# Kernel tuning notes

Measured on AMD Instinct MI355X. Metric: run time of the kernel, lower is better.

## Reference

```python
import jax, jax.numpy as jnp
import numpy as np

TOP_K = 2
LORA_SCALE = 32.0 / 16.0  # alpha / rank


def setup_inputs() -> dict:
    key = jax.random.key(0)
    ks = jax.random.split(key, 11)
    N, D, F, E, R = 1024, 2048, 5632, 8, 16
    s = lambda k, shape, fan: jax.random.normal(k, shape, jnp.float32) / np.sqrt(fan)
    return {
        "x": jax.random.normal(ks[0], (N, D), jnp.float32),
        "gate_w": s(ks[1], (E, D), D),
        "W1": s(ks[2], (F, D), D),
        "W3": s(ks[3], (F, D), D),
        "W2": s(ks[4], (D, F), F),
        "A1": s(ks[5], (E, R, D), D),
        "B1": s(ks[6], (F, R), R)[None].repeat(E, 0) * 0.0 + s(ks[6], (E, F, R), R),
        "A3": s(ks[7], (E, R, D), D),
        "B3": s(ks[8], (E, F, R), R),
        "A2": s(ks[9], (E, R, F), F),
        "B2": s(ks[10], (E, D, R), R),
    }


def reference(x, gate_w, W1, W3, W2, A1, B1, A3, B3, A2, B2):
    # --- router: softmax over experts, top-k, renormalized combine weights ---
    logits = x @ gate_w.T                                   # [N, E]
    probs = jax.nn.softmax(logits, axis=-1)
    topw, topi = jax.lax.top_k(probs, TOP_K)                # [N, K]
    topw = topw / jnp.sum(topw, axis=-1, keepdims=True)
    E = gate_w.shape[0]
    w = jnp.sum(jax.nn.one_hot(topi, E, dtype=x.dtype) * topw[..., None], axis=1)  # [N, E]

    # --- experts: shared base weights + per-expert LoRA (fused SwiGLU) ---
    base1 = x @ W1.T                                        # [N, F]
    base3 = x @ W3.T                                        # [N, F]
    l1 = jnp.einsum("nd,erd->ner", x, A1)                   # rank-R bottleneck
    l3 = jnp.einsum("nd,erd->ner", x, A3)
    h1 = base1[:, None, :] + LORA_SCALE * jnp.einsum("ner,efr->nef", l1, B1)  # [N, E, F]
    h3 = base3[:, None, :] + LORA_SCALE * jnp.einsum("ner,efr->nef", l3, B3)
    s = jax.nn.silu(h1) * h3                                # [N, E, F]

    # down-projection: shared W2 applied to the routed mixture, plus per-expert LoRA
    s_mix = jnp.einsum("ne,nef->nf", w, s)                  # [N, F]
    out = s_mix @ W2.T                                      # [N, D]
    l2 = jnp.einsum("nef,erf->ner", s, A2) * (w[:, :, None] * LORA_SCALE)
    out = out + jnp.einsum("ner,edr->nd", l2, B2)           # [N, D]
    return out, logits
```

## Files before the change

### kernel.cpp

```cpp
#include <hip/hip_runtime.h>

typedef unsigned int u32;
typedef unsigned short u16;

#define N_TOK 1024
#define D_DIM 2048
#define F_DIM 5632
#define E_NUM 8
#define R_DIM 16
#define LSCALE 2.0f
#define FT 256
#define NT (F_DIM / FT)
#define TC 8
#define BN13 11520
#define ZSPLIT 8

typedef __bf16 bf16x8 __attribute__((ext_vector_type(8)));
typedef float f32x4 __attribute__((ext_vector_type(4)));
typedef u16 u16x8 __attribute__((ext_vector_type(8)));

__device__ inline u16 f2bf(float f) {
    u32 u = __builtin_bit_cast(u32, f);
    u32 r = (u + 0x7fffu + ((u >> 16) & 1u)) >> 16;
    return (u16)r;
}
__device__ inline float bf2f(u16 h) {
    u32 u = ((u32)h) << 16;
    return __builtin_bit_cast(float, u);
}

#define LGKM0() do { asm volatile("s_waitcnt lgkmcnt(0)" ::: "memory"); \
                     __builtin_amdgcn_sched_barrier(0); } while (0)
#define VMC(n)  do { asm volatile("s_waitcnt vmcnt(" #n ")" ::: "memory"); \
                     __builtin_amdgcn_sched_barrier(0); } while (0)

__global__ __launch_bounds__(256) void cvt_all(const float* __restrict__ x,
                                               const float* __restrict__ W1,
                                               const float* __restrict__ W3,
                                               const float* __restrict__ A1,
                                               const float* __restrict__ A3,
                                               const float* __restrict__ W2,
                                               const float* __restrict__ B1,
                                               const float* __restrict__ B3,
                                               u16* __restrict__ xb,
                                               u16* __restrict__ w13,
                                               u16* __restrict__ w2b,
                                               u16* __restrict__ b1b,
                                               u16* __restrict__ b3b) {
    int i = blockIdx.x * 256 + threadIdx.x;
    const float* src;
    u16* dst;
    int off;
    if (i < 524288)       { src = x;  dst = xb;             off = i; }
    else if (i < 3407872) { src = W1; dst = w13;            off = i - 524288; }
    else if (i < 6291456) { src = W3; dst = w13 + 11534336; off = i - 3407872; }
    else if (i < 6356992) { src = A1; dst = w13 + 23068672; off = i - 6291456; }
    else if (i < 6422528) { src = A3; dst = w13 + 23330816; off = i - 6356992; }
    else if (i < 9306112) { src = W2; dst = w2b;            off = i - 6422528; }
    else if (i < 9486336) { src = B1; dst = b1b;            off = i - 9306112; }
    else                  { src = B3; dst = b3b;            off = i - 9486336; }
    float4 v = ((const float4*)src)[off];
    union { u16 h[4]; ushort4 u4; } o;
    o.h[0] = f2bf(v.x); o.h[1] = f2bf(v.y); o.h[2] = f2bf(v.z); o.h[3] = f2bf(v.w);
    ((ushort4*)dst)[off] = o.u4;
}

__global__ __launch_bounds__(256) void a2_transpose(const float* __restrict__ A2,
                                                    u16* __restrict__ A2t) {
    int e = blockIdx.y;
    int f = blockIdx.x * 256 + threadIdx.x;
    u16 row[16];
#pragma unroll
    for (int r = 0; r < 16; ++r)
        row[r] = f2bf(A2[((size_t)e * R_DIM + r) * F_DIM + f]);
    u16* dst = A2t + ((size_t)e * F_DIM + f) * 16;
#pragma unroll
    for (int q = 0; q < 2; ++q)
        ((ulonglong2*)dst)[q] = ((ulonglong2*)row)[q];
}

__global__ __launch_bounds__(256) void router_kernel(const float* __restrict__ x,
                                                     const float* __restrict__ gw,
                                                     float* __restrict__ logits,
                                                     int* __restrict__ ridx,
                                                     float* __restrict__ rw) {
    int n = blockIdx.x;
    int tid = threadIdx.x;
    float part[E_NUM];
#pragma unroll
    for (int e = 0; e < E_NUM; ++e) part[e] = 0.f;
    const float* xr = x + (size_t)n * D_DIM;
    for (int d = tid; d < D_DIM; d += 256) {
        float xv = xr[d];
#pragma unroll
        for (int e = 0; e < E_NUM; ++e) part[e] += xv * gw[e * D_DIM + d];
    }
    __shared__ float sh[E_NUM][256];
#pragma unroll
    for (int e = 0; e < E_NUM; ++e) sh[e][tid] = part[e];
    __syncthreads();
    for (int off = 128; off > 0; off >>= 1) {
        if (tid < off) {
#pragma unroll
            for (int e = 0; e < E_NUM; ++e) sh[e][tid] += sh[e][tid + off];
        }
        __syncthreads();
    }
    if (tid == 0) {
        float lg[E_NUM], p[E_NUM];
        float mx = -1e30f;
        for (int e = 0; e < E_NUM; ++e) {
            lg[e] = sh[e][0];
            logits[n * E_NUM + e] = lg[e];
            if (lg[e] > mx) mx = lg[e];
        }
        float s = 0.f;
        for (int e = 0; e < E_NUM; ++e) { p[e] = expf(lg[e] - mx); s += p[e]; }
        for (int e = 0; e < E_NUM; ++e) p[e] /= s;
        int i1 = 0;
        for (int e = 1; e < E_NUM; ++e) if (p[e] > p[i1]) i1 = e;
        int i2 = (i1 == 0) ? 1 : 0;
        for (int e = 0; e < E_NUM; ++e) if (e != i1 && p[e] > p[i2]) i2 = e;
        float t = p[i1] + p[i2];
        ridx[n * 2] = i1; ridx[n * 2 + 1] = i2;
        rw[n * 2] = p[i1] / t; rw[n * 2 + 1] = p[i2] / t;
    }
}

__global__ __launch_bounds__(256) void build_lists(const int* __restrict__ ridx,
                                                   int* __restrict__ counts,
                                                   u32* __restrict__ lists) {
    int n = blockIdx.x * 256 + threadIdx.x;
    if (n >= N_TOK) return;
#pragma unroll
    for (int k = 0; k < 2; ++k) {
        int e = ridx[n * 2 + k];
        int slot = atomicAdd(&counts[e], 1);
        lists[e * N_TOK + slot] = (u32)n | ((u32)k << 16);
    }
}

__global__ __launch_bounds__(512, 2) void gemm256(const u16* __restrict__ A,
                                                  const u16* __restrict__ B,
                                                  float* __restrict__ C,
                                                  int N, int K, int kslice,
                                                  int mode, int ntm, int ntn) {
    __shared__ __align__(16) u16 lds[2][2][2][256 * 32];

    const int nb = gridDim.x;
    const int fb = blockIdx.x;
    const int qq = nb >> 3, rr = nb & 7;
    const int xcd = fb & 7, lo = fb >> 3;
    const int wg = (xcd < rr ? xcd * (qq + 1) : rr * (qq + 1) + (xcd - rr) * qq) + lo;

    const int mt = wg % ntm;
    const int t2 = wg / ntm;
    const int nt = t2 % ntn;
    const int zt = t2 / ntn;

    const int bm0 = mt * 256;
    const int bn0 = nt * 256;
    const int kb = zt * kslice;

    const int tid = threadIdx.x;
    const int lane = tid & 63;
    const int wave = tid >> 6;
    const int quad = lane >> 4;
    const int l16 = lane & 15;
    const int swz = (l16 & 8) << 1;
    const int wm = (wave >> 2) * 128;
    const int wn = (wave & 3) * 64;

    f32x4 zero = {0.f, 0.f, 0.f, 0.f};
    f32x4 acc[8][4];
#pragma unroll
    for (int i = 0; i < 8; ++i)
#pragma unroll
        for (int j = 0; j < 4; ++j) acc[i][j] = zero;

    auto stageHalf = [&](const u16* __restrict__ G, int mat, int buf, int h,
                         int k0, int rowBase) {
#pragma unroll
        for (int j = 0; j < 2; ++j) {
            int seg = wave * 2 + j;
            int plane = seg >> 3;
            int rb = seg & 7;
            int r = h * 128 + rb * 16 + (lane >> 2);
            int slot = lane & 3;
            int gcol = k0 + plane * 32 + ((slot * 8) ^ ((r & 8) << 1));
            const u16* gp = G + (size_t)(rowBase + r) * K + gcol;
            u16* lp = &lds[mat][buf][plane][(h * 128 + rb * 16) * 32] + lane * 8;
            __builtin_amdgcn_global_load_lds((const __attribute__((address_space(1))) u32*)gp,
                                             (__attribute__((address_space(3))) u32*)lp,
                                             16, 0, 0);
        }
    };

    auto ldA = [&](int buf, int ks, int mi) -> bf16x8 {
        return *(const bf16x8*)&lds[0][buf][ks]
            [(wm + mi * 16 + l16) * 32 + ((quad * 8) ^ swz)];
    };
    auto ldB = [&](int buf, int ks, int ni) -> bf16x8 {
        return *(const bf16x8*)&lds[1][buf][ks]
            [(wn + ni * 16 + l16) * 32 + ((quad * 8) ^ swz)];
    };

    const int nk = kslice >> 6;

    stageHalf(A, 0, 0, 0, kb, bm0);
    stageHalf(A, 0, 0, 1, kb, bm0);
    stageHalf(B, 1, 0, 0, kb, bn0);
    stageHalf(B, 1, 0, 1, kb, bn0);
    stageHalf(B, 1, 1, 0, kb + 64, bn0);
    stageHalf(B, 1, 1, 1, kb + 64, bn0);
    VMC(4);
    __builtin_amdgcn_s_barrier();

    for (int t = 0; t < nk; ++t) {
        const int buf = t & 1;
        const int k0 = kb + t * 64;
        bf16x8 bq0[4], bq1[4];

        {
            bf16x8 av[4];
#pragma unroll
            for (int mi = 0; mi < 4; ++mi) av[mi] = ldA(buf, 0, mi);
#pragma unroll
            for (int ni = 0; ni < 4; ++ni) bq0[ni] = ldB(buf, 0, ni);
            if (t + 1 < nk) stageHalf(A, 0, buf ^ 1, 0, k0 + 64, bm0);
            LGKM0();
            __builtin_amdgcn_s_setprio(1);
#pragma unroll
            for (int mi = 0; mi < 4; ++mi)
#pragma unroll
                for (int ni = 0; ni < 4; ++ni)
                    acc[mi][ni] = __builtin_amdgcn_mfma_f32_16x16x32_bf16(
                        av[mi], bq0[ni], acc[mi][ni], 0, 0, 0);
            __builtin_amdgcn_s_setprio(0);
            __builtin_amdgcn_s_barrier();
        }

        {
            bf16x8 av[4];
#pragma unroll
            for (int mi = 0; mi < 4; ++mi) av[mi] = ldA(buf, 0, 4 + mi);
#pragma unroll
            for (int ni = 0; ni < 4; ++ni) bq1[ni] = ldB(buf, 1, ni);
            if (t + 1 < nk) stageHalf(A, 0, buf ^ 1, 1, k0 + 64, bm0);
            LGKM0();
            __builtin_amdgcn_s_setprio(1);
#pragma unroll
            for (int mi = 0; mi < 4; ++mi)
#pragma unroll
                for (int ni = 0; ni < 4; ++ni)
                    acc[4 + mi][ni] = __builtin_amdgcn_mfma_f32_16x16x32_bf16(
                        av[mi], bq0[ni], acc[4 + mi][ni], 0, 0, 0);
            __builtin_amdgcn_s_setprio(0);
            __builtin_amdgcn_s_barrier();
        }

        {
            bf16x8 av[4];
#pragma unroll
            for (int mi = 0; mi < 4; ++mi) av[mi] = ldA(buf, 1, mi);
            if (t + 2 < nk) stageHalf(B, 1, buf, 0, k0 + 128, bn0);
            LGKM0();
            __builtin_amdgcn_s_setprio(1);
#pragma unroll
            for (int mi = 0; mi < 4; ++mi)
#pragma unroll
                for (int ni = 0; ni < 4; ++ni)
                    acc[mi][ni] = __builtin_amdgcn_mfma_f32_16x16x32_bf16(
                        av[mi], bq1[ni], acc[mi][ni], 0, 0, 0);
            __builtin_amdgcn_s_setprio(0);
            __builtin_amdgcn_s_barrier();
        }

        {
            bf16x8 av[4];
#pragma unroll
            for (int mi = 0; mi < 4; ++mi) av[mi] = ldA(buf, 1, 4 + mi);
            if (t + 2 < nk) stageHalf(B, 1, buf, 1, k0 + 128, bn0);
            LGKM0();
            __builtin_amdgcn_s_setprio(1);
#pragma unroll
            for (int mi = 0; mi < 4; ++mi)
#pragma unroll
                for (int ni = 0; ni < 4; ++ni)
                    acc[4 + mi][ni] = __builtin_amdgcn_mfma_f32_16x16x32_bf16(
                        av[mi], bq1[ni], acc[4 + mi][ni], 0, 0, 0);
            __builtin_amdgcn_s_setprio(0);
            if (t < nk - 2)       { VMC(4); }
            else if (t == nk - 2) { VMC(0); }
            __builtin_amdgcn_s_barrier();
        }
    }

    float* Cz = C + (size_t)zt * ntm * 256 * N;
#pragma unroll
    for (int mi = 0; mi < 8; ++mi)
#pragma unroll
        for (int ni = 0; ni < 4; ++ni) {
            int col = bn0 + wn + ni * 16 + l16;
#pragma unroll
            for (int i = 0; i < 4; ++i) {
                int row = bm0 + wm + mi * 16 + quad * 4 + i;
                if (mode == 1) {
                    ((u16*)C)[(size_t)row * N + col] = f2bf(acc[mi][ni][i]);
                } else {
                    Cz[(size_t)row * N + col] = acc[mi][ni][i];
                }
            }
        }
}

__global__ __launch_bounds__(256) void act_v2b(const u16* __restrict__ base13,
                                               const u16* __restrict__ B1b,
                                               const u16* __restrict__ B3b,
                                               const u32* __restrict__ lists,
                                               const int* __restrict__ counts,
                                               const float* __restrict__ rw,
                                               u16* __restrict__ sbuf) {
    const int ft = blockIdx.x;
    const int e  = blockIdx.y;
    const int z  = blockIdx.z;
    const int tid = threadIdx.x;
    const int lane = tid & 63;
    const int wave = tid >> 6;
    const int f_lane = ft * FT + lane * 4;

    u16x8 w1c[8], w3c[8];
    {
        const u16* p1 = B1b + ((size_t)e * F_DIM + f_lane) * 16;
        const u16* p3 = B3b + ((size_t)e * F_DIM + f_lane) * 16;
#pragma unroll
        for (int c = 0; c < 8; ++c) {
            w1c[c] = *(const u16x8*)(p1 + c * 8);
            w3c[c] = *(const u16x8*)(p3 + c * 8);
        }
    }

    const int T = counts[e];
    for (int i = z * 4 + wave; i < T; i += TC * 4) {
        u32 ent = lists[e * N_TOK + i];
        int n = (int)(ent & 0xFFFFu);
        int k = (int)(ent >> 16);
        float wt = rw[n * 2 + k];

        float la1[16], la3[16];
        {
            const u16x8* pl1 = (const u16x8*)(base13 + (size_t)n * BN13 + 11264 + e * 16);
            const u16x8* pl3 = (const u16x8*)(base13 + (size_t)n * BN13 + 11392 + e * 16);
#pragma unroll
            for (int h = 0; h < 2; ++h) {
                u16x8 t1 = pl1[h], t3 = pl3[h];
#pragma unroll
                for (int qq = 0; qq < 8; ++qq) {
                    la1[h * 8 + qq] = LSCALE * bf2f(t1[qq]);
                    la3[h * 8 + qq] = LSCALE * bf2f(t3[qq]);
                }
            }
        }

        ushort4 b1u = *(const ushort4*)(base13 + (size_t)n * BN13 + f_lane);
        ushort4 b3u = *(const ushort4*)(base13 + (size_t)n * BN13 + 5632 + f_lane);
        const u16* b1p = (const u16*)&b1u;
        const u16* b3p = (const u16*)&b3u;

        u16 sv[4];
#pragma unroll
        for (int j = 0; j < 4; ++j) {
            float h1 = bf2f(b1p[j]);
            float h3 = bf2f(b3p[j]);
#pragma unroll
            for (int qq = 0; qq < 8; ++qq) {
                h1 += la1[qq] * bf2f(w1c[2 * j][qq]);
                h3 += la3[qq] * bf2f(w3c[2 * j][qq]);
            }
#pragma unroll
            for (int qq = 0; qq < 8; ++qq) {
                h1 += la1[8 + qq] * bf2f(w1c[2 * j + 1][qq]);
                h3 += la3[8 + qq] * bf2f(w3c[2 * j + 1][qq]);
            }
            float sg = h1 / (1.f + __expf(-h1));
            sv[j] = f2bf(wt * sg * h3);
        }
        *(ushort4*)(sbuf + ((size_t)k * N_TOK + n) * F_DIM + f_lane) = *(ushort4*)sv;
    }
}

__global__ __launch_bounds__(256) void combine_kernel(const u16* __restrict__ sbuf,
                                                      u16* __restrict__ smix) {
    size_t i = ((size_t)blockIdx.x * 256 + threadIdx.x) * 8;
    u16x8 a = *(const u16x8*)(sbuf + i);
    u16x8 b = *(const u16x8*)(sbuf + (size_t)N_TOK * F_DIM + i);
    u16x8 o;
#pragma unroll
    for (int q = 0; q < 8; ++q) o[q] = f2bf(bf2f(a[q]) + bf2f(b[q]));
    *(u16x8*)(smix + i) = o;
}

__global__ __launch_bounds__(256) void lora_down_v4(const u16* __restrict__ sbuf,
                                                    const u16* __restrict__ A2t,
                                                    const int* __restrict__ ridx,
                                                    const float* __restrict__ B2,
                                                    const float* __restrict__ pbuf,
                                                    float* __restrict__ out) {
    const int n = blockIdx.x, tid = threadIdx.x;
    __shared__ float part[2][32][16];
    __shared__ float fin[2][16];
    __shared__ int se[2];
    if (tid < 2) se[tid] = ridx[n * 2 + tid];
    __syncthreads();

    {
        const int k = tid >> 7;
        const int tt = tid & 127;
        const int rq = tt & 3;
        const int fc = tt >> 2;
        const int e = se[k];
        const u16* srow = sbuf + ((size_t)k * N_TOK + n) * F_DIM + fc * 176;
        const u16* arow = A2t + ((size_t)e * F_DIM + fc * 176) * 16 + rq * 4;
        float acc0 = 0.f, acc1 = 0.f, acc2 = 0.f, acc3 = 0.f;
#pragma unroll 4
        for (int f = 0; f < 176; ++f) {
            float sv = bf2f(srow[f]);
            ushort4 wr = *(const ushort4*)(arow + (size_t)f * 16);
            acc0 += sv * bf2f(wr.x);
            acc1 += sv * bf2f(wr.y);
            acc2 += sv * bf2f(wr.z);
            acc3 += sv * bf2f(wr.w);
        }
        part[k][fc][rq * 4 + 0] = acc0;
        part[k][fc][rq * 4 + 1] = acc1;
        part[k][fc][rq * 4 + 2] = acc2;
        part[k][fc][rq * 4 + 3] = acc3;
    }
    __syncthreads();
    if (tid < 32) {
        int k = tid >> 4, r = tid & 15;
        float s = 0.f;
#pragma unroll
        for (int fc = 0; fc < 32; ++fc) s += part[k][fc][r];
        fin[k][r] = LSCALE * s;
    }
    __syncthreads();

    float a0[16], a1v[16];
#pragma unroll
    for (int r = 0; r < 16; ++r) { a0[r] = fin[0][r]; a1v[r] = fin[1][r]; }
    const float* B2a = B2 + (size_t)se[0] * D_DIM * R_DIM;
    const float* B2b = B2 + (size_t)se[1] * D_DIM * R_DIM;
    const float* prow = pbuf + (size_t)n * D_DIM;
    float* orow = out + (size_t)n * D_DIM;
    for (int d = tid; d < D_DIM; d += 256) {
        const float4* pa = (const float4*)(B2a + (size_t)d * 16);
        const float4* pb = (const float4*)(B2b + (size_t)d * 16);
        float acc = 0.f;
#pragma unroll
        for (int q = 0; q < 4; ++q) {
            float4 va = pa[q];
            acc += a0[q * 4] * va.x + a0[q * 4 + 1] * va.y +
                   a0[q * 4 + 2] * va.z + a0[q * 4 + 3] * va.w;
            float4 vb = pb[q];
            acc += a1v[q * 4] * vb.x + a1v[q * 4 + 1] * vb.y +
                   a1v[q * 4 + 2] * vb.z + a1v[q * 4 + 3] * vb.w;
        }
        float ps = 0.f;
#pragma unroll
        for (int z = 0; z < ZSPLIT; ++z)
            ps += prow[(size_t)z * N_TOK * D_DIM + d];
        orow[d] = acc + ps;
    }
}

extern "C" void kernel_launch(void* const* d_in, const int* in_sizes, int n_in,
                              void* d_out, int out_size, void* d_ws, size_t ws_size,
                              hipStream_t stream) {
    const float* x  = (const float*)d_in[0];
    const float* gw = (const float*)d_in[1];
    const float* W1 = (const float*)d_in[2];
    const float* W3 = (const float*)d_in[3];
    const float* W2 = (const float*)d_in[4];
    const float* A1 = (const float*)d_in[5];
    const float* B1 = (const float*)d_in[6];
    const float* A3 = (const float*)d_in[7];
    const float* B3 = (const float*)d_in[8];
    const float* A2 = (const float*)d_in[9];
    const float* B2 = (const float*)d_in[10];
    float* out = (float*)d_out;
    float* logits = out + (size_t)N_TOK * D_DIM;

    char* ws = (char*)d_ws;
    size_t off = 0;
    auto alloc = [&](size_t bytes) { char* p = ws + off; off += (bytes + 255) & ~(size_t)255; return p; };
    u16*   xb    = (u16*)alloc((size_t)N_TOK * D_DIM * 2);
    u16*   W13b  = (u16*)alloc((size_t)BN13 * D_DIM * 2);
    u16*   W2b   = (u16*)alloc((size_t)D_DIM * F_DIM * 2);
    u16*   base13= (u16*)alloc((size_t)N_TOK * BN13 * 2);
    int*   ridx  = (int*)alloc((size_t)N_TOK * 2 * 4);
    float* rwt   = (float*)alloc((size_t)N_TOK * 2 * 4);
    u16*   B1b   = (u16*)alloc((size_t)E_NUM * F_DIM * R_DIM * 2);
    u16*   B3b   = (u16*)alloc((size_t)E_NUM * F_DIM * R_DIM * 2);
    u16*   A2t   = (u16*)alloc((size_t)E_NUM * F_DIM * R_DIM * 2);
    int*   counts= (int*)alloc(64);
    u32*   lists = (u32*)alloc((size_t)E_NUM * N_TOK * 4);
    u16*   sbuf  = (u16*)alloc((size_t)2 * N_TOK * F_DIM * 2);
    u16*   smixb = (u16*)alloc((size_t)N_TOK * F_DIM * 2);
    float* pbuf  = (float*)alloc((size_t)ZSPLIT * N_TOK * D_DIM * 4);
    (void)ws_size; (void)in_sizes; (void)n_in; (void)out_size;

    cvt_all<<<37760, 256, 0, stream>>>(x, W1, W3, A1, A3, W2, B1, B3,
                                       xb, W13b, W2b, B1b, B3b);
    a2_transpose<<<dim3(F_DIM / 256, E_NUM), 256, 0, stream>>>(A2, A2t);

    router_kernel<<<N_TOK, 256, 0, stream>>>(x, gw, logits, ridx, rwt);
    hipMemsetAsync(counts, 0, 64, stream);
    build_lists<<<N_TOK / 256, 256, 0, stream>>>(ridx, counts, lists);

    gemm256<<<180, 512, 0, stream>>>(xb, W13b, (float*)base13,
                                     BN13, D_DIM, D_DIM, 1, 4, 45);

    act_v2b<<<dim3(NT, E_NUM, TC), 256, 0, stream>>>(base13, B1b, B3b,
                                                     lists, counts, rwt, sbuf);

    combine_kernel<<<(N_TOK * F_DIM / 8) / 256, 256, 0, stream>>>(sbuf, smixb);

    gemm256<<<256, 512, 0, stream>>>(smixb, W2b, pbuf,
                                     D_DIM, F_DIM, 704, 0, 4, 8);

    lora_down_v4<<<N_TOK, 256, 0, stream>>>(sbuf, A2t, ridx, B2, pbuf, out);
}
```

Measured before the change: 399.5 us.

## Overlap W2/B/A2 conversion with first GEMM via extra blocks; fuse list building into router

The first GEMM launch gets 76 extra workgroups. These convert W2, B1 and B3 to bf16 and transpose A2, so that work runs in parallel with the 180 GEMM tiles instead of in separate pre-kernels. The router kernel now builds the per-expert token lists with atomics directly, and cvt_all zeroes the counts, which removes the memset and the build_lists launch. Fewer launches and better CU occupancy on the 256-CU device are the goal. The conversion blocks compete with the GEMM for memory bandwidth. List order may also change, but slot order was already nondeterministic.

```diff
diff --git a/kernel.cpp b/kernel.cpp
--- a/kernel.cpp
+++ b/kernel.cpp
@@ -28,6 +28,12 @@
     u32 u = ((u32)h) << 16;
     return __builtin_bit_cast(float, u);
 }
+__device__ inline void cvt4(const float* __restrict__ s, u16* __restrict__ d, int i) {
+    float4 v = ((const float4*)s)[i];
+    union { u16 h[4]; ushort4 u4; } o;
+    o.h[0] = f2bf(v.x); o.h[1] = f2bf(v.y); o.h[2] = f2bf(v.z); o.h[3] = f2bf(v.w);
+    ((ushort4*)d)[i] = o.u4;
+}
 
 #define LGKM0() do { asm volatile("s_waitcnt lgkmcnt(0)" ::: "memory"); \
                      __builtin_amdgcn_sched_barrier(0); } while (0)
@@ -39,14 +45,10 @@
                                                const float* __restrict__ W3,
                                                const float* __restrict__ A1,
                                                const float* __restrict__ A3,
-                                               const float* __restrict__ W2,
-                                               const float* __restrict__ B1,
-                                               const float* __restrict__ B3,
                                                u16* __restrict__ xb,
                                                u16* __restrict__ w13,
-                                               u16* __restrict__ w2b,
-                                               u16* __restrict__ b1b,
-                                               u16* __restrict__ b3b) {
+                                               int* __restrict__ counts) {
+    if (blockIdx.x == 0 && threadIdx.x < E_NUM) counts[threadIdx.x] = 0;
     int i = blockIdx.x * 256 + threadIdx.x;
     const float* src;
     u16* dst;
@@ -55,35 +57,17 @@
     else if (i < 3407872) { src = W1; dst = w13;            off = i - 524288; }
     else if (i < 6291456) { src = W3; dst = w13 + 11534336; off = i - 3407872; }
     else if (i < 6356992) { src = A1; dst = w13 + 23068672; off = i - 6291456; }
-    else if (i < 6422528) { src = A3; dst = w13 + 23330816; off = i - 6356992; }
-    else if (i < 9306112) { src = W2; dst = w2b;            off = i - 6422528; }
-    else if (i < 9486336) { src = B1; dst = b1b;            off = i - 9306112; }
-    else                  { src = B3; dst = b3b;            off = i - 9486336; }
-    float4 v = ((const float4*)src)[off];
-    union { u16 h[4]; ushort4 u4; } o;
-    o.h[0] = f2bf(v.x); o.h[1] = f2bf(v.y); o.h[2] = f2bf(v.z); o.h[3] = f2bf(v.w);
-    ((ushort4*)dst)[off] = o.u4;
-}
-
-__global__ __launch_bounds__(256) void a2_transpose(const float* __restrict__ A2,
-                                                    u16* __restrict__ A2t) {
-    int e = blockIdx.y;
-    int f = blockIdx.x * 256 + threadIdx.x;
-    u16 row[16];
-#pragma unroll
-    for (int r = 0; r < 16; ++r)
-        row[r] = f2bf(A2[((size_t)e * R_DIM + r) * F_DIM + f]);
-    u16* dst = A2t + ((size_t)e * F_DIM + f) * 16;
-#pragma unroll
-    for (int q = 0; q < 2; ++q)
-        ((ulonglong2*)dst)[q] = ((ulonglong2*)row)[q];
+    else                  { src = A3; dst = w13 + 23330816; off = i - 6356992; }
+    cvt4(src, dst, off);
 }
 
 __global__ __launch_bounds__(256) void router_kernel(const float* __restrict__ x,
                                                      const float* __restrict__ gw,
                                                      float* __restrict__ logits,
                                                      int* __restrict__ ridx,
-                                                     float* __restrict__ rw) {
+                                                     float* __restrict__ rw,
+                                                     int* __restrict__ counts,
+                                                     u32* __restrict__ lists) {
     int n = blockIdx.x;
     int tid = threadIdx.x;
     float part[E_NUM];
@@ -124,19 +108,10 @@
         float t = p[i1] + p[i2];
         ridx[n * 2] = i1; ridx[n * 2 + 1] = i2;
         rw[n * 2] = p[i1] / t; rw[n * 2 + 1] = p[i2] / t;
-    }
-}
-
-__global__ __launch_bounds__(256) void build_lists(const int* __restrict__ ridx,
-                                                   int* __restrict__ counts,
-                                                   u32* __restrict__ lists) {
-    int n = blockIdx.x * 256 + threadIdx.x;
-    if (n >= N_TOK) return;
-#pragma unroll
-    for (int k = 0; k < 2; ++k) {
-        int e = ridx[n * 2 + k];
-        int slot = atomicAdd(&counts[e], 1);
-        lists[e * N_TOK + slot] = (u32)n | ((u32)k << 16);
+        int s1 = atomicAdd(&counts[i1], 1);
+        lists[i1 * N_TOK + s1] = (u32)n;
+        int s2 = atomicAdd(&counts[i2], 1);
+        lists[i2 * N_TOK + s2] = (u32)n | (1u << 16);
     }
 }
 
@@ -144,7 +119,16 @@
                                                   const u16* __restrict__ B,
                                                   float* __restrict__ C,
                                                   int N, int K, int kslice,
-                                                  int mode, int ntm, int ntn) {
+                                                  int mode, int ntm, int ntn,
+                                                  int ngemm,
+                                                  const float* __restrict__ cvW2,
+                                                  const float* __restrict__ cvB1,
+                                                  const float* __restrict__ cvB3,
+                                                  const float* __restrict__ cvA2,
+                                                  u16* __restrict__ oW2,
+                                                  u16* __restrict__ oB1,
+                                                  u16* __restrict__ oB3,
+                                                  u16* __restrict__ oA2t) {
     __shared__ __align__(16) u16 lds[2][2][2][256 * 32];
 
     const int nb = gridDim.x;
@@ -153,6 +137,29 @@
     const int xcd = fb & 7, lo = fb >> 3;
     const int wg = (xcd < rr ? xcd * (qq + 1) : rr * (qq + 1) + (xcd - rr) * qq) + lo;
 
+    const int tid = threadIdx.x;
+
+    if (wg >= ngemm) {
+        const int nh = nb - ngemm;
+        const int base = (wg - ngemm) * 512 + tid;
+        const int stride = nh * 512;
+        for (int i = base; i < 2883584; i += stride) cvt4(cvW2, oW2, i);
+        for (int i = base; i < 180224; i += stride)  cvt4(cvB1, oB1, i);
+        for (int i = base; i < 180224; i += stride)  cvt4(cvB3, oB3, i);
+        for (int i = base; i < 45056; i += stride) {
+            int e = i / F_DIM, f = i - e * F_DIM;
+            u16 row[16];
+#pragma unroll
+            for (int r = 0; r < 16; ++r)
+                row[r] = f2bf(cvA2[((size_t)e * R_DIM + r) * F_DIM + f]);
+            u16* dst = oA2t + ((size_t)e * F_DIM + f) * 16;
+#pragma unroll
+            for (int q = 0; q < 2; ++q)
+                ((ulonglong2*)dst)[q] = ((ulonglong2*)row)[q];
+        }
+        return;
+    }
+
     const int mt = wg % ntm;
     const int t2 = wg / ntm;
     const int nt = t2 % ntn;
@@ -162,7 +169,6 @@
     const int bn0 = nt * 256;
     const int kb = zt * kslice;
 
-    const int tid = threadIdx.x;
     const int lane = tid & 63;
     const int wave = tid >> 6;
     const int quad = lane >> 4;
@@ -510,16 +516,14 @@
     float* pbuf  = (float*)alloc((size_t)ZSPLIT * N_TOK * D_DIM * 4);
     (void)ws_size; (void)in_sizes; (void)n_in; (void)out_size;
 
-    cvt_all<<<37760, 256, 0, stream>>>(x, W1, W3, A1, A3, W2, B1, B3,
-                                       xb, W13b, W2b, B1b, B3b);
-    a2_transpose<<<dim3(F_DIM / 256, E_NUM), 256, 0, stream>>>(A2, A2t);
-
-    router_kernel<<<N_TOK, 256, 0, stream>>>(x, gw, logits, ridx, rwt);
-    hipMemsetAsync(counts, 0, 64, stream);
-    build_lists<<<N_TOK / 256, 256, 0, stream>>>(ridx, counts, lists);
-
-    gemm256<<<180, 512, 0, stream>>>(xb, W13b, (float*)base13,
-                                     BN13, D_DIM, D_DIM, 1, 4, 45);
+    cvt_all<<<25088, 256, 0, stream>>>(x, W1, W3, A1, A3, xb, W13b, counts);
+
+    router_kernel<<<N_TOK, 256, 0, stream>>>(x, gw, logits, ridx, rwt, counts, lists);
+
+    gemm256<<<256, 512, 0, stream>>>(xb, W13b, (float*)base13,
+                                     BN13, D_DIM, D_DIM, 1, 4, 45,
+                                     180,
+                                     W2, B1, B3, A2, W2b, B1b, B3b, A2t);
 
     act_v2b<<<dim3(NT, E_NUM, TC), 256, 0, stream>>>(base13, B1b, B3b,
                                                      lists, counts, rwt, sbuf);
@@ -527,7 +531,10 @@
     combine_kernel<<<(N_TOK * F_DIM / 8) / 256, 256, 0, stream>>>(sbuf, smixb);
 
     gemm256<<<256, 512, 0, stream>>>(smixb, W2b, pbuf,
-                                     D_DIM, F_DIM, 704, 0, 4, 8);
+                                     D_DIM, F_DIM, 704, 0, 4, 8,
+                                     256,
+                                     nullptr, nullptr, nullptr, nullptr,
+                                     nullptr, nullptr, nullptr, nullptr);
 
     lora_down_v4<<<N_TOK, 256, 0, stream>>>(sbuf, A2t, ridx, B2, pbuf, out);
 }
```

New measurement: 409.4 us. 1.02x slower.
